# Kernel optimization log

Measured on AMD Instinct MI355X. Metric: run time of the kernel, lower is better.

## Reference

```python
import jax, jax.numpy as jnp
import numpy as np

B = 262144      # batch
DIN = 100       # input covariate dim (cfg_density[0][0])
H = 64          # hidden dim
G = 10          # num_grid -> density output dim G+1
NH = 5          # number of dosage-bucket heads in Multi_head


def setup_inputs() -> dict:
    key = jax.random.key(0)
    ks = jax.random.split(key, 16)
    s = 0.05
    return {
        "dosage": jax.random.uniform(ks[0], (B,), dtype=jnp.float32),
        "x": jax.random.normal(ks[1], (B, DIN), dtype=jnp.float32),
        # density feature MLP (two Linear+ReLU layers)
        "dW0": jax.random.normal(ks[2], (DIN, H), dtype=jnp.float32) * s,
        "db0": jax.random.normal(ks[3], (H,), dtype=jnp.float32) * s,
        "dW1": jax.random.normal(ks[4], (H, H), dtype=jnp.float32) * s,
        "db1": jax.random.normal(ks[5], (H,), dtype=jnp.float32) * s,
        # Density_Block: Linear(H -> G+1) then softmax + grid interpolation
        "dbW": jax.random.normal(ks[6], (H, G + 1), dtype=jnp.float32) * s,
        "dbB": jax.random.normal(ks[7], (G + 1,), dtype=jnp.float32) * s,
        # Multi_head: 5 structurally identical heads, params stacked on axis 0
        # layer0: Treat_Linear(64 -> 64, relu, istreat=1)
        "W0": jax.random.normal(ks[8], (NH, H, H), dtype=jnp.float32) * s,
        "tw0": jax.random.normal(ks[9], (NH, H), dtype=jnp.float32) * s,
        "b0": jax.random.normal(ks[10], (NH, H), dtype=jnp.float32) * s,
        # layer1 (last): Treat_Linear(64 -> 1, no act, istreat=1)
        "W1": jax.random.normal(ks[11], (NH, H, 1), dtype=jnp.float32) * s,
        "tw1": jax.random.normal(ks[12], (NH, 1), dtype=jnp.float32) * s,
        "b1": jax.random.normal(ks[13], (NH, 1), dtype=jnp.float32) * s,
    }


def reference(dosage, x, dW0, db0, dW1, db1, dbW, dbB, W0, tw0, b0, W1, tw1, b1):
    # hidden feature MLP
    hidden = jax.nn.relu(x @ dW0 + db0)
    hidden = jax.nn.relu(hidden @ dW1 + db1)            # [B, H]

    # ---- Density_Block: softmax over grid, dual gather + linear interpolation
    p = jax.nn.softmax(hidden @ dbW + dbB, axis=1)      # [B, G+1]
    tB = dosage * G
    U = jnp.ceil(tB)
    inter = 1.0 - (U - tB)                              # fractional position in cell
    Ui = U.astype(jnp.int32)
    Li = Ui - 1
    Li = Li + (Li < 0).astype(jnp.int32)                # clamp L=-1 -> 0
    pL = jnp.take_along_axis(p, Li[:, None], axis=1)[:, 0]
    pU = jnp.take_along_axis(p, Ui[:, None], axis=1)[:, 0]
    g = pL + (pU - pL) * inter                          # [B]

    # ---- Multi_head: 5 heads on dosage buckets [0,.2),[.2,.4),...,[.8,1.)
    t = dosage
    # layer0: out = feat @ W + t * tw + b, relu; compute all heads, select later
    h0 = jax.nn.relu(
        jnp.einsum('bi,hio->bho', hidden, W0)
        + t[:, None, None] * tw0[None]
        + b0[None]
    )                                                   # [B, NH, H]
    # last layer: no activation
    out1 = (jnp.einsum('bho,hoj->bhj', h0, W1)
            + t[:, None, None] * tw1[None]
            + b1[None])                                 # [B, NH, 1]
    bucket = jnp.clip(jnp.floor(t * NH).astype(jnp.int32), 0, NH - 1)
    Q = jnp.take_along_axis(out1, bucket[:, None, None], axis=1)[:, 0, :]  # [B, 1]
    return g, Q
```

## Files before the change

### kernel.cpp

```cpp
#include <hip/hip_runtime.h>

typedef __attribute__((ext_vector_type(8))) short  short8;
typedef __attribute__((ext_vector_type(4))) float  floatx4;
typedef __attribute__((ext_vector_type(4))) int    intx4;

constexpr int DIN = 100;
constexpr int H   = 64;
constexpr int G   = 10;
constexpr int NH  = 5;
constexpr int MWG = 128;
constexpr int HP  = 72;

constexpr int NF_DW0 = 16, NF_DW1 = 8, NF_DBW = 2;
constexpr int NF_LIN = NF_DW0 + NF_DW1 + NF_DBW;
constexpr int NF_TOT = NF_LIN + 40;

__device__ __forceinline__ unsigned short f2bf_rne(float f) {
    union { float f; unsigned u; } v{f};
    unsigned r = v.u + 0x7FFF + ((v.u >> 16) & 1);
    return (unsigned short)(r >> 16);
}

__device__ __forceinline__ short8 pack8(const float* f) {
    intx4 p;
    #pragma unroll
    for (int j = 0; j < 4; ++j) {
        unsigned a = __float_as_uint(f[2 * j])     + 0x8000u;
        unsigned b = __float_as_uint(f[2 * j + 1]) + 0x8000u;
        p[j] = (int)((b & 0xFFFF0000u) | (a >> 16));
    }
    union { intx4 i; short8 s; } u; u.i = p;
    return u.s;
}

__device__ __forceinline__ unsigned short f2bf_hu(float f) {
    return (unsigned short)((__float_as_uint(f) + 0x8000u) >> 16);
}

__device__ __forceinline__ short8 ldfrag(const unsigned short* __restrict__ ws,
                                         int f, int lane) {
    return *(const short8*)(ws + (size_t)(f * 64 + lane) * 8);
}

__global__ __launch_bounds__(64) void pack_kernel(
    const float* __restrict__ dW0, const float* __restrict__ dW1,
    const float* __restrict__ dbW, const float* __restrict__ W0,
    unsigned short* __restrict__ ws)
{
    const int f = blockIdx.x;
    const int lane = threadIdx.x;
    const int q = lane >> 4, cl = lane & 15;
    float v[8];
    if (f < NF_DW0) {
        int c = f >> 2, g = f & 3;
        #pragma unroll
        for (int j = 0; j < 8; ++j) {
            int k = c * 32 + q * 8 + j, n = g * 16 + cl;
            v[j] = (k < DIN) ? dW0[k * H + n] : 0.0f;
        }
    } else if (f < NF_DW0 + NF_DW1) {
        int r = f - NF_DW0; int c = r >> 2, g = r & 3;
        #pragma unroll
        for (int j = 0; j < 8; ++j) {
            int k = c * 32 + q * 8 + j, n = g * 16 + cl;
            v[j] = dW1[k * H + n];
        }
    } else if (f < NF_LIN) {
        int c = f - (NF_DW0 + NF_DW1);
        #pragma unroll
        for (int j = 0; j < 8; ++j) {
            int k = c * 32 + q * 8 + j, n = cl;
            v[j] = (n <= G) ? dbW[k * (G + 1) + n] : 0.0f;
        }
    } else {
        int r = f - NF_LIN; int h = r >> 3; r &= 7; int c = r >> 2, g = r & 3;
        #pragma unroll
        for (int j = 0; j < 8; ++j) {
            int k = c * 32 + q * 8 + j, n = g * 16 + cl;
            v[j] = W0[(h * H + k) * H + n];
        }
    }
    short8 s;
    #pragma unroll
    for (int j = 0; j < 8; ++j) s[j] = (short)f2bf_rne(v[j]);
    *(short8*)(ws + (size_t)(f * 64 + lane) * 8) = s;
}

__global__ __launch_bounds__(256) void drnet_mfma(
    const float* __restrict__ dosage, const float* __restrict__ x,
    const float* __restrict__ db0, const float* __restrict__ db1,
    const float* __restrict__ dbB,
    const float* __restrict__ tw0, const float* __restrict__ b0,
    const float* __restrict__ W1, const float* __restrict__ tw1,
    const float* __restrict__ b1,
    const unsigned short* __restrict__ wsfrag,
    float* __restrict__ outg, float* __restrict__ outq)
{
    __shared__ unsigned short hbuf[MWG * HP];
    const int tid  = threadIdx.x;
    const int wave = tid >> 6, lane = tid & 63;
    const int q = lane >> 4, cl = lane & 15;
    const int rowbase = blockIdx.x * MWG + wave * 32;
    unsigned short* hb = hbuf + wave * 32 * HP;

    float t8[2][4];
    int   bk8[2][4];
    #pragma unroll
    for (int mt = 0; mt < 2; ++mt)
        #pragma unroll
        for (int r = 0; r < 4; ++r) {
            float t = dosage[rowbase + mt * 16 + 4 * q + r];
            t8[mt][r] = t;
            int bk = (int)floorf(t * (float)NH);
            bk8[mt][r] = min(max(bk, 0), NH - 1);
        }

    floatx4 acc[2][4];

    short8 a1[2][4];
    #pragma unroll
    for (int mt = 0; mt < 2; ++mt) {
        const float* xr = x + (size_t)(rowbase + mt * 16 + cl) * DIN;
        #pragma unroll
        for (int cch = 0; cch < 4; ++cch) {
            float f[8];
            if (cch < 3) {
                floatx4 u0 = *(const floatx4*)(xr + cch * 32 + q * 8);
                floatx4 u1 = *(const floatx4*)(xr + cch * 32 + q * 8 + 4);
                f[0]=u0.x; f[1]=u0.y; f[2]=u0.z; f[3]=u0.w;
                f[4]=u1.x; f[5]=u1.y; f[6]=u1.z; f[7]=u1.w;
            } else {
                if (q == 0) {
                    floatx4 u0 = *(const floatx4*)(xr + 96);
                    f[0]=u0.x; f[1]=u0.y; f[2]=u0.z; f[3]=u0.w;
                    f[4]=f[5]=f[6]=f[7]=0.0f;
                } else {
                    #pragma unroll
                    for (int j = 0; j < 8; ++j) f[j] = 0.0f;
                }
            }
            a1[mt][cch] = pack8(f);
        }
    }
    #pragma unroll
    for (int mt = 0; mt < 2; ++mt)
        #pragma unroll
        for (int g = 0; g < 4; ++g) acc[mt][g] = (floatx4)0.0f;
    #pragma unroll
    for (int cch = 0; cch < 4; ++cch)
        #pragma unroll
        for (int g = 0; g < 4; ++g) {
            short8 bf = ldfrag(wsfrag, cch * 4 + g, lane);
            #pragma unroll
            for (int mt = 0; mt < 2; ++mt)
                acc[mt][g] = __builtin_amdgcn_mfma_f32_16x16x32_bf16(a1[mt][cch], bf, acc[mt][g], 0, 0, 0);
        }
    #pragma unroll
    for (int g = 0; g < 4; ++g) {
        float bias = db0[g * 16 + cl];
        #pragma unroll
        for (int mt = 0; mt < 2; ++mt)
            #pragma unroll
            for (int r = 0; r < 4; ++r)
                hb[(mt * 16 + 4 * q + r) * HP + g * 16 + cl] =
                    f2bf_hu(fmaxf(acc[mt][g][r] + bias, 0.0f));
    }

    short8 a2[2][2];
    #pragma unroll
    for (int mt = 0; mt < 2; ++mt)
        #pragma unroll
        for (int cch = 0; cch < 2; ++cch)
            a2[mt][cch] = *(const short8*)(hb + (mt * 16 + cl) * HP + cch * 32 + q * 8);
    #pragma unroll
    for (int mt = 0; mt < 2; ++mt)
        #pragma unroll
        for (int g = 0; g < 4; ++g) acc[mt][g] = (floatx4)0.0f;
    #pragma unroll
    for (int cch = 0; cch < 2; ++cch)
        #pragma unroll
        for (int g = 0; g < 4; ++g) {
            short8 bf = ldfrag(wsfrag, NF_DW0 + cch * 4 + g, lane);
            #pragma unroll
            for (int mt = 0; mt < 2; ++mt)
                acc[mt][g] = __builtin_amdgcn_mfma_f32_16x16x32_bf16(a2[mt][cch], bf, acc[mt][g], 0, 0, 0);
        }
    #pragma unroll
    for (int g = 0; g < 4; ++g) {
        float bias = db1[g * 16 + cl];
        #pragma unroll
        for (int mt = 0; mt < 2; ++mt)
            #pragma unroll
            for (int r = 0; r < 4; ++r)
                hb[(mt * 16 + 4 * q + r) * HP + g * 16 + cl] =
                    f2bf_hu(fmaxf(acc[mt][g][r] + bias, 0.0f));
    }

    short8 af[2][2];
    #pragma unroll
    for (int mt = 0; mt < 2; ++mt)
        #pragma unroll
        for (int cch = 0; cch < 2; ++cch)
            af[mt][cch] = *(const short8*)(hb + (mt * 16 + cl) * HP + cch * 32 + q * 8);

    floatx4 accd[2];
    accd[0] = (floatx4)0.0f; accd[1] = (floatx4)0.0f;
    #pragma unroll
    for (int cch = 0; cch < 2; ++cch) {
        short8 bf = ldfrag(wsfrag, NF_DW0 + NF_DW1 + cch, lane);
        #pragma unroll
        for (int mt = 0; mt < 2; ++mt)
            accd[mt] = __builtin_amdgcn_mfma_f32_16x16x32_bf16(af[mt][cch], bf, accd[mt], 0, 0, 0);
    }
    const float dbBv = (cl <= G) ? dbB[cl] : 0.0f;
    float gout[2][4];
    #pragma unroll
    for (int mt = 0; mt < 2; ++mt)
        #pragma unroll
        for (int r = 0; r < 4; ++r) {
            float l = (cl <= G) ? (accd[mt][r] + dbBv) : -1e30f;
            float m = l;
            m = fmaxf(m, __shfl_xor(m, 1)); m = fmaxf(m, __shfl_xor(m, 2));
            m = fmaxf(m, __shfl_xor(m, 4)); m = fmaxf(m, __shfl_xor(m, 8));
            float e = __expf(l - m);
            float s = e;
            s += __shfl_xor(s, 1); s += __shfl_xor(s, 2);
            s += __shfl_xor(s, 4); s += __shfl_xor(s, 8);
            const float t  = t8[mt][r];
            const float tB = t * (float)G;
            const float U  = ceilf(tB);
            const float inter = 1.0f - (U - tB);
            int Ui = (int)U; int Li = Ui - 1; if (Li < 0) Li = 0;
            float pL = __shfl(e, q * 16 + Li);
            float pU = __shfl(e, q * 16 + Ui);
            gout[mt][r] = (pL + (pU - pL) * inter) / s;
        }
    if (cl == 0) {
        #pragma unroll
        for (int mt = 0; mt < 2; ++mt) {
            floatx4 gv = { gout[mt][0], gout[mt][1], gout[mt][2], gout[mt][3] };
            *(floatx4*)(outg + rowbase + mt * 16 + 4 * q) = gv;
        }
    }

    float asel[2][4][4];
    #pragma unroll
    for (int mt = 0; mt < 2; ++mt)
        #pragma unroll
        for (int g = 0; g < 4; ++g)
            #pragma unroll
            for (int r = 0; r < 4; ++r) asel[mt][g][r] = 0.0f;

    #pragma unroll 1
    for (int h = 0; h < NH; ++h) {
        floatx4 acch[2][4];
        #pragma unroll
        for (int mt = 0; mt < 2; ++mt)
            #pragma unroll
            for (int g = 0; g < 4; ++g) acch[mt][g] = (floatx4)0.0f;
        #pragma unroll
        for (int cch = 0; cch < 2; ++cch)
            #pragma unroll
            for (int g = 0; g < 4; ++g) {
                short8 bf = ldfrag(wsfrag, NF_LIN + h * 8 + cch * 4 + g, lane);
                #pragma unroll
                for (int mt = 0; mt < 2; ++mt)
                    acch[mt][g] = __builtin_amdgcn_mfma_f32_16x16x32_bf16(af[mt][cch], bf, acch[mt][g], 0, 0, 0);
            }
        #pragma unroll
        for (int mt = 0; mt < 2; ++mt)
            #pragma unroll
            for (int r = 0; r < 4; ++r) {
                bool sel = (bk8[mt][r] == h);
                #pragma unroll
                for (int g = 0; g < 4; ++g)
                    asel[mt][g][r] = sel ? acch[mt][g][r] : asel[mt][g][r];
            }
    }

    float qp[2][4] = {{0,0,0,0},{0,0,0,0}};
    #pragma unroll
    for (int g = 0; g < 4; ++g) {
        const int ci = g * 16 + cl;
        #pragma unroll
        for (int mt = 0; mt < 2; ++mt)
            #pragma unroll
            for (int r = 0; r < 4; ++r) {
                const int off = bk8[mt][r] * H + ci;
                float h0 = asel[mt][g][r] + t8[mt][r] * tw0[off] + b0[off];
                qp[mt][r] += fmaxf(h0, 0.0f) * W1[off];
            }
    }
    #pragma unroll
    for (int mt = 0; mt < 2; ++mt)
        #pragma unroll
        for (int r = 0; r < 4; ++r) {
            float s = qp[mt][r];
            s += __shfl_xor(s, 1); s += __shfl_xor(s, 2);
            s += __shfl_xor(s, 4); s += __shfl_xor(s, 8);
            const int h = bk8[mt][r];
            qp[mt][r] = s + t8[mt][r] * tw1[h] + b1[h];
        }
    if (cl == 0) {
        #pragma unroll
        for (int mt = 0; mt < 2; ++mt) {
            floatx4 Qv = { qp[mt][0], qp[mt][1], qp[mt][2], qp[mt][3] };
            *(floatx4*)(outq + rowbase + mt * 16 + 4 * q) = Qv;
        }
    }
}

extern "C" void kernel_launch(void* const* d_in, const int* in_sizes, int n_in,
                              void* d_out, int out_size, void* d_ws, size_t ws_size,
                              hipStream_t stream) {
    const float* dosage = (const float*)d_in[0];
    const float* x      = (const float*)d_in[1];
    const float* dW0    = (const float*)d_in[2];
    const float* db0    = (const float*)d_in[3];
    const float* dW1    = (const float*)d_in[4];
    const float* db1    = (const float*)d_in[5];
    const float* dbW    = (const float*)d_in[6];
    const float* dbB    = (const float*)d_in[7];
    const float* W0     = (const float*)d_in[8];
    const float* tw0    = (const float*)d_in[9];
    const float* b0     = (const float*)d_in[10];
    const float* W1     = (const float*)d_in[11];
    const float* tw1    = (const float*)d_in[12];
    const float* b1     = (const float*)d_in[13];

    const int Btot = in_sizes[0];
    float* outg = (float*)d_out;
    float* outq = outg + Btot;
    unsigned short* ws = (unsigned short*)d_ws;

    pack_kernel<<<NF_TOT, 64, 0, stream>>>(dW0, dW1, dbW, W0, ws);
    drnet_mfma<<<Btot / MWG, 256, 0, stream>>>(dosage, x, db0, db1, dbB,
                                               tw0, b0, W1, tw1, b1,
                                               ws, outg, outq);
}
```

Before: 229.4 us.

## Cut register pressure: fold head epilogue into loop, vectorize dosage loads

Adds a min-blocks-per-CU hint of 4 to launch bounds and scopes temporaries so they die early. The head loop now computes each head's relu, dot with W1 and masked accumulation per iteration, replacing the 32-float asel selection buffer and the per-row gathered loads of tw0/b0/W1 with uniform per-head loads. Dosage is read with a vector load. This aims to lower VGPR use and raise occupancy, at the cost of doing the epilogue arithmetic for all five heads and risking spills under the tighter register budget.

```diff
diff --git a/kernel.cpp b/kernel.cpp
--- a/kernel.cpp
+++ b/kernel.cpp
@@ -86,7 +86,7 @@
     *(short8*)(ws + (size_t)(f * 64 + lane) * 8) = s;
 }
 
-__global__ __launch_bounds__(256) void drnet_mfma(
+__global__ __launch_bounds__(256, 4) void drnet_mfma(
     const float* __restrict__ dosage, const float* __restrict__ x,
     const float* __restrict__ db0, const float* __restrict__ db1,
     const float* __restrict__ dbB,
@@ -106,55 +106,59 @@
     float t8[2][4];
     int   bk8[2][4];
     #pragma unroll
-    for (int mt = 0; mt < 2; ++mt)
+    for (int mt = 0; mt < 2; ++mt) {
+        floatx4 tv = *(const floatx4*)(dosage + rowbase + mt * 16 + 4 * q);
         #pragma unroll
         for (int r = 0; r < 4; ++r) {
-            float t = dosage[rowbase + mt * 16 + 4 * q + r];
+            float t = tv[r];
             t8[mt][r] = t;
             int bk = (int)floorf(t * (float)NH);
             bk8[mt][r] = min(max(bk, 0), NH - 1);
         }
+    }
 
     floatx4 acc[2][4];
 
-    short8 a1[2][4];
-    #pragma unroll
-    for (int mt = 0; mt < 2; ++mt) {
-        const float* xr = x + (size_t)(rowbase + mt * 16 + cl) * DIN;
-        #pragma unroll
-        for (int cch = 0; cch < 4; ++cch) {
-            float f[8];
-            if (cch < 3) {
-                floatx4 u0 = *(const floatx4*)(xr + cch * 32 + q * 8);
-                floatx4 u1 = *(const floatx4*)(xr + cch * 32 + q * 8 + 4);
-                f[0]=u0.x; f[1]=u0.y; f[2]=u0.z; f[3]=u0.w;
-                f[4]=u1.x; f[5]=u1.y; f[6]=u1.z; f[7]=u1.w;
-            } else {
-                if (q == 0) {
-                    floatx4 u0 = *(const floatx4*)(xr + 96);
+    {
+        short8 a1[2][4];
+        #pragma unroll
+        for (int mt = 0; mt < 2; ++mt) {
+            const float* xr = x + (size_t)(rowbase + mt * 16 + cl) * DIN;
+            #pragma unroll
+            for (int cch = 0; cch < 4; ++cch) {
+                float f[8];
+                if (cch < 3) {
+                    floatx4 u0 = *(const floatx4*)(xr + cch * 32 + q * 8);
+                    floatx4 u1 = *(const floatx4*)(xr + cch * 32 + q * 8 + 4);
                     f[0]=u0.x; f[1]=u0.y; f[2]=u0.z; f[3]=u0.w;
-                    f[4]=f[5]=f[6]=f[7]=0.0f;
+                    f[4]=u1.x; f[5]=u1.y; f[6]=u1.z; f[7]=u1.w;
                 } else {
-                    #pragma unroll
-                    for (int j = 0; j < 8; ++j) f[j] = 0.0f;
+                    if (q == 0) {
+                        floatx4 u0 = *(const floatx4*)(xr + 96);
+                        f[0]=u0.x; f[1]=u0.y; f[2]=u0.z; f[3]=u0.w;
+                        f[4]=f[5]=f[6]=f[7]=0.0f;
+                    } else {
+                        #pragma unroll
+                        for (int j = 0; j < 8; ++j) f[j] = 0.0f;
+                    }
                 }
-            }
-            a1[mt][cch] = pack8(f);
-        }
-    }
-    #pragma unroll
-    for (int mt = 0; mt < 2; ++mt)
-        #pragma unroll
-        for (int g = 0; g < 4; ++g) acc[mt][g] = (floatx4)0.0f;
-    #pragma unroll
-    for (int cch = 0; cch < 4; ++cch)
-        #pragma unroll
-        for (int g = 0; g < 4; ++g) {
-            short8 bf = ldfrag(wsfrag, cch * 4 + g, lane);
-            #pragma unroll
-            for (int mt = 0; mt < 2; ++mt)
-                acc[mt][g] = __builtin_amdgcn_mfma_f32_16x16x32_bf16(a1[mt][cch], bf, acc[mt][g], 0, 0, 0);
-        }
+                a1[mt][cch] = pack8(f);
+            }
+        }
+        #pragma unroll
+        for (int mt = 0; mt < 2; ++mt)
+            #pragma unroll
+            for (int g = 0; g < 4; ++g) acc[mt][g] = (floatx4)0.0f;
+        #pragma unroll
+        for (int cch = 0; cch < 4; ++cch)
+            #pragma unroll
+            for (int g = 0; g < 4; ++g) {
+                short8 bf = ldfrag(wsfrag, cch * 4 + g, lane);
+                #pragma unroll
+                for (int mt = 0; mt < 2; ++mt)
+                    acc[mt][g] = __builtin_amdgcn_mfma_f32_16x16x32_bf16(a1[mt][cch], bf, acc[mt][g], 0, 0, 0);
+            }
+    }
     #pragma unroll
     for (int g = 0; g < 4; ++g) {
         float bias = db0[g * 16 + cl];
@@ -166,25 +170,27 @@
                     f2bf_hu(fmaxf(acc[mt][g][r] + bias, 0.0f));
     }
 
-    short8 a2[2][2];
-    #pragma unroll
-    for (int mt = 0; mt < 2; ++mt)
+    {
+        short8 a2[2][2];
+        #pragma unroll
+        for (int mt = 0; mt < 2; ++mt)
+            #pragma unroll
+            for (int cch = 0; cch < 2; ++cch)
+                a2[mt][cch] = *(const short8*)(hb + (mt * 16 + cl) * HP + cch * 32 + q * 8);
+        #pragma unroll
+        for (int mt = 0; mt < 2; ++mt)
+            #pragma unroll
+            for (int g = 0; g < 4; ++g) acc[mt][g] = (floatx4)0.0f;
         #pragma unroll
         for (int cch = 0; cch < 2; ++cch)
-            a2[mt][cch] = *(const short8*)(hb + (mt * 16 + cl) * HP + cch * 32 + q * 8);
-    #pragma unroll
-    for (int mt = 0; mt < 2; ++mt)
-        #pragma unroll
-        for (int g = 0; g < 4; ++g) acc[mt][g] = (floatx4)0.0f;
-    #pragma unroll
-    for (int cch = 0; cch < 2; ++cch)
-        #pragma unroll
-        for (int g = 0; g < 4; ++g) {
-            short8 bf = ldfrag(wsfrag, NF_DW0 + cch * 4 + g, lane);
-            #pragma unroll
-            for (int mt = 0; mt < 2; ++mt)
-                acc[mt][g] = __builtin_amdgcn_mfma_f32_16x16x32_bf16(a2[mt][cch], bf, acc[mt][g], 0, 0, 0);
-        }
+            #pragma unroll
+            for (int g = 0; g < 4; ++g) {
+                short8 bf = ldfrag(wsfrag, NF_DW0 + cch * 4 + g, lane);
+                #pragma unroll
+                for (int mt = 0; mt < 2; ++mt)
+                    acc[mt][g] = __builtin_amdgcn_mfma_f32_16x16x32_bf16(a2[mt][cch], bf, acc[mt][g], 0, 0, 0);
+            }
+    }
     #pragma unroll
     for (int g = 0; g < 4; ++g) {
         float bias = db1[g * 16 + cl];
@@ -203,54 +209,47 @@
         for (int cch = 0; cch < 2; ++cch)
             af[mt][cch] = *(const short8*)(hb + (mt * 16 + cl) * HP + cch * 32 + q * 8);
 
-    floatx4 accd[2];
-    accd[0] = (floatx4)0.0f; accd[1] = (floatx4)0.0f;
-    #pragma unroll
-    for (int cch = 0; cch < 2; ++cch) {
-        short8 bf = ldfrag(wsfrag, NF_DW0 + NF_DW1 + cch, lane);
-        #pragma unroll
-        for (int mt = 0; mt < 2; ++mt)
-            accd[mt] = __builtin_amdgcn_mfma_f32_16x16x32_bf16(af[mt][cch], bf, accd[mt], 0, 0, 0);
-    }
-    const float dbBv = (cl <= G) ? dbB[cl] : 0.0f;
-    float gout[2][4];
-    #pragma unroll
-    for (int mt = 0; mt < 2; ++mt)
-        #pragma unroll
-        for (int r = 0; r < 4; ++r) {
-            float l = (cl <= G) ? (accd[mt][r] + dbBv) : -1e30f;
-            float m = l;
-            m = fmaxf(m, __shfl_xor(m, 1)); m = fmaxf(m, __shfl_xor(m, 2));
-            m = fmaxf(m, __shfl_xor(m, 4)); m = fmaxf(m, __shfl_xor(m, 8));
-            float e = __expf(l - m);
-            float s = e;
-            s += __shfl_xor(s, 1); s += __shfl_xor(s, 2);
-            s += __shfl_xor(s, 4); s += __shfl_xor(s, 8);
-            const float t  = t8[mt][r];
-            const float tB = t * (float)G;
-            const float U  = ceilf(tB);
-            const float inter = 1.0f - (U - tB);
-            int Ui = (int)U; int Li = Ui - 1; if (Li < 0) Li = 0;
-            float pL = __shfl(e, q * 16 + Li);
-            float pU = __shfl(e, q * 16 + Ui);
-            gout[mt][r] = (pL + (pU - pL) * inter) / s;
-        }
-    if (cl == 0) {
+    {
+        floatx4 accd[2];
+        accd[0] = (floatx4)0.0f; accd[1] = (floatx4)0.0f;
+        #pragma unroll
+        for (int cch = 0; cch < 2; ++cch) {
+            short8 bf = ldfrag(wsfrag, NF_DW0 + NF_DW1 + cch, lane);
+            #pragma unroll
+            for (int mt = 0; mt < 2; ++mt)
+                accd[mt] = __builtin_amdgcn_mfma_f32_16x16x32_bf16(af[mt][cch], bf, accd[mt], 0, 0, 0);
+        }
+        const float dbBv = (cl <= G) ? dbB[cl] : 0.0f;
         #pragma unroll
         for (int mt = 0; mt < 2; ++mt) {
-            floatx4 gv = { gout[mt][0], gout[mt][1], gout[mt][2], gout[mt][3] };
-            *(floatx4*)(outg + rowbase + mt * 16 + 4 * q) = gv;
-        }
-    }
-
-    float asel[2][4][4];
-    #pragma unroll
-    for (int mt = 0; mt < 2; ++mt)
-        #pragma unroll
-        for (int g = 0; g < 4; ++g)
-            #pragma unroll
-            for (int r = 0; r < 4; ++r) asel[mt][g][r] = 0.0f;
-
+            float gout[4];
+            #pragma unroll
+            for (int r = 0; r < 4; ++r) {
+                float l = (cl <= G) ? (accd[mt][r] + dbBv) : -1e30f;
+                float m = l;
+                m = fmaxf(m, __shfl_xor(m, 1)); m = fmaxf(m, __shfl_xor(m, 2));
+                m = fmaxf(m, __shfl_xor(m, 4)); m = fmaxf(m, __shfl_xor(m, 8));
+                float e = __expf(l - m);
+                float s = e;
+                s += __shfl_xor(s, 1); s += __shfl_xor(s, 2);
+                s += __shfl_xor(s, 4); s += __shfl_xor(s, 8);
+                const float t  = t8[mt][r];
+                const float tB = t * (float)G;
+                const float U  = ceilf(tB);
+                const float inter = 1.0f - (U - tB);
+                int Ui = (int)U; int Li = Ui - 1; if (Li < 0) Li = 0;
+                float pL = __shfl(e, q * 16 + Li);
+                float pU = __shfl(e, q * 16 + Ui);
+                gout[r] = (pL + (pU - pL) * inter) / s;
+            }
+            if (cl == 0) {
+                floatx4 gv = { gout[0], gout[1], gout[2], gout[3] };
+                *(floatx4*)(outg + rowbase + mt * 16 + 4 * q) = gv;
+            }
+        }
+    }
+
+    float qp[2][4] = {{0,0,0,0},{0,0,0,0}};
     #pragma unroll 1
     for (int h = 0; h < NH; ++h) {
         floatx4 acch[2][4];
@@ -267,32 +266,27 @@
                 for (int mt = 0; mt < 2; ++mt)
                     acch[mt][g] = __builtin_amdgcn_mfma_f32_16x16x32_bf16(af[mt][cch], bf, acch[mt][g], 0, 0, 0);
             }
+        float tw0g[4], b0g[4], w1g[4];
+        #pragma unroll
+        for (int g = 0; g < 4; ++g) {
+            const int off = h * H + g * 16 + cl;
+            tw0g[g] = tw0[off]; b0g[g] = b0[off]; w1g[g] = W1[off];
+        }
         #pragma unroll
         for (int mt = 0; mt < 2; ++mt)
             #pragma unroll
             for (int r = 0; r < 4; ++r) {
-                bool sel = (bk8[mt][r] == h);
+                float s = 0.0f;
                 #pragma unroll
-                for (int g = 0; g < 4; ++g)
-                    asel[mt][g][r] = sel ? acch[mt][g][r] : asel[mt][g][r];
-            }
-    }
-
-    float qp[2][4] = {{0,0,0,0},{0,0,0,0}};
-    #pragma unroll
-    for (int g = 0; g < 4; ++g) {
-        const int ci = g * 16 + cl;
-        #pragma unroll
-        for (int mt = 0; mt < 2; ++mt)
-            #pragma unroll
-            for (int r = 0; r < 4; ++r) {
-                const int off = bk8[mt][r] * H + ci;
-                float h0 = asel[mt][g][r] + t8[mt][r] * tw0[off] + b0[off];
-                qp[mt][r] += fmaxf(h0, 0.0f) * W1[off];
-            }
-    }
-    #pragma unroll
-    for (int mt = 0; mt < 2; ++mt)
+                for (int g = 0; g < 4; ++g) {
+                    float h0 = acch[mt][g][r] + t8[mt][r] * tw0g[g] + b0g[g];
+                    s += fmaxf(h0, 0.0f) * w1g[g];
+                }
+                qp[mt][r] += (bk8[mt][r] == h) ? s : 0.0f;
+            }
+    }
+    #pragma unroll
+    for (int mt = 0; mt < 2; ++mt) {
         #pragma unroll
         for (int r = 0; r < 4; ++r) {
             float s = qp[mt][r];
@@ -301,9 +295,7 @@
             const int h = bk8[mt][r];
             qp[mt][r] = s + t8[mt][r] * tw1[h] + b1[h];
         }
-    if (cl == 0) {
-        #pragma unroll
-        for (int mt = 0; mt < 2; ++mt) {
+        if (cl == 0) {
             floatx4 Qv = { qp[mt][0], qp[mt][1], qp[mt][2], qp[mt][3] };
             *(floatx4*)(outq + rowbase + mt * 16 + 4 * q) = Qv;
         }
```

After: 203.2 us. 11.4% less time.
